# Kernel optimization log

Hardware: AMD Instinct MI355X
Metric: run time of the kernel (lower is better)

The kernel has to match this reference:

```python
import jax, jax.numpy as jnp
import numpy as np

N, T, D, H = 32, 2048, 256, 256


def setup_inputs() -> dict:
    key = jax.random.key(0)
    k0, k1, k2, k3, k4 = jax.random.split(key, 5)
    std = 1.0 / np.sqrt(H + D)  # matches PTLSTM.reset()
    return {
        "x": jax.random.normal(k0, (N, T, D), dtype=jnp.float32),
        "state": jnp.zeros((N, 2 * H), dtype=jnp.float32),  # [h0 | c0]
        "w_ih": (jax.random.normal(k1, (4 * H, D)) * std).astype(jnp.float32),
        "w_hh": (jax.random.normal(k2, (4 * H, H)) * std).astype(jnp.float32),
        "b_ih": (jax.random.normal(k3, (4 * H,)) * std).astype(jnp.float32),
        "b_hh": (jax.random.normal(k4, (4 * H,)) * std).astype(jnp.float32),
    }


def reference(x, state, w_ih, w_hh, b_ih, b_hh):
    # Single-layer batch_first LSTM, PyTorch gate order (i, f, g, o).
    Hd = w_hh.shape[1]
    h0, c0 = state[:, :Hd], state[:, Hd:]
    # Precompute input-to-hidden projection for all timesteps (one big GEMM).
    xg = jnp.einsum('ntd,gd->ntg', x, w_ih) + (b_ih + b_hh)  # [N, T, 4H]

    def step(carry, xg_t):
        h, c = carry
        gates = xg_t + h @ w_hh.T  # [N, 4H]
        i, f, g, o = jnp.split(gates, 4, axis=-1)
        i = jax.nn.sigmoid(i)
        f = jax.nn.sigmoid(f)
        g = jnp.tanh(g)
        o = jax.nn.sigmoid(o)
        c = f * c + i * g
        h = o * jnp.tanh(c)
        return (h, c), h

    (hT, cT), out_t = jax.lax.scan(step, (h0, c0), jnp.swapaxes(xg, 0, 1))
    output = jnp.swapaxes(out_t, 0, 1)  # [N, T, H]
    outstate = jnp.concatenate([hT, cT], axis=1)  # [N, 2H]
    return output, outstate
```

## Files before the change

kernel.cpp:

```cpp
#include <hip/hip_runtime.h>

typedef _Float16 half2_t __attribute__((ext_vector_type(2)));
typedef __bf16   bf16x8  __attribute__((ext_vector_type(8)));
typedef float    f32x4   __attribute__((ext_vector_type(4)));
typedef unsigned short u16x8 __attribute__((ext_vector_type(8)));
typedef unsigned int  uint32;
typedef unsigned long long uint64;

#define LSTM_N 32
#define LSTM_T 2048
#define LSTM_D 256
#define LSTM_H 256
#define NG 1024
#define CH 256
#define NCH (LSTM_T / CH)
#define MCH (LSTM_N * CH)

#define OFF_XG   ((size_t)0)
#define SZ_XG    ((size_t)MCH * NG * 4)
#define OFF_WIHB (OFF_XG + SZ_XG)
#define SZ_WIHB  ((size_t)NG * LSTM_D * 2)
#define OFF_BIAS (OFF_WIHB + SZ_WIHB)
#define SZ_BIAS  ((size_t)4096)
#define OFF_WPK  (OFF_BIAS + SZ_BIAS)
#define SZ_WPK   ((size_t)4 * 512 * 64 * 4)
#define OFF_CST  (OFF_WPK + SZ_WPK)
#define SZ_CST   ((size_t)LSTM_N * 256 * 4)
#define OFF_HX   (OFF_CST + SZ_CST)
#define SZ_HX    ((size_t)LSTM_N * 2 * 128 * 8)

#if defined(__has_builtin)
#if __has_builtin(__builtin_amdgcn_fdot2)
#define HAVE_FDOT2 1
#endif
#endif

__device__ __forceinline__ float fdot2(uint32 w, uint32 h, float acc) {
#ifdef HAVE_FDOT2
  return __builtin_amdgcn_fdot2(__builtin_bit_cast(half2_t, w),
                                __builtin_bit_cast(half2_t, h), acc, false);
#else
  half2_t wv = __builtin_bit_cast(half2_t, w);
  half2_t hv = __builtin_bit_cast(half2_t, h);
  float r = fmaf((float)wv.x, (float)hv.x, acc);
  return fmaf((float)wv.y, (float)hv.y, r);
#endif
}

__device__ __forceinline__ float sigm(float x) { return 1.f / (1.f + __expf(-x)); }
__device__ __forceinline__ float tanh_fast(float x) { return 2.f / (1.f + __expf(-2.f * x)) - 1.f; }

__device__ __forceinline__ unsigned short f2bf(float f) {
  uint32 u = __builtin_bit_cast(uint32, f);
  uint32 r = (u + 0x7FFFu + ((u >> 16) & 1u)) >> 16;
  return (unsigned short)r;
}

__device__ __forceinline__ float bfly8(const float a[8], int kap) {
  float k0[4], g0[4];
  const bool b4 = (kap & 4) != 0;
#pragma unroll
  for (int v = 0; v < 4; ++v) {
    k0[v] = b4 ? a[v + 4] : a[v];
    g0[v] = b4 ? a[v] : a[v + 4];
  }
#pragma unroll
  for (int v = 0; v < 4; ++v) k0[v] += __shfl_xor(g0[v], 4, 64);
  float k1[2], g1[2];
  const bool b2 = (kap & 2) != 0;
#pragma unroll
  for (int v = 0; v < 2; ++v) {
    k1[v] = b2 ? k0[v + 2] : k0[v];
    g1[v] = b2 ? k0[v] : k0[v + 2];
  }
#pragma unroll
  for (int v = 0; v < 2; ++v) k1[v] += __shfl_xor(g1[v], 2, 64);
  const bool b1 = (kap & 1) != 0;
  float k2 = b1 ? k1[1] : k1[0];
  float g2 = b1 ? k1[0] : k1[1];
  return k2 + __shfl_xor(g2, 1, 64);
}


__global__ void cvt_bf16_k(const float* __restrict__ src, unsigned short* __restrict__ dst, int n) {
  int i = blockIdx.x * blockDim.x + threadIdx.x;
  if (4 * i + 3 < n) {
    float4 v = ((const float4*)src)[i];
    ushort4 o;
    o.x = f2bf(v.x); o.y = f2bf(v.y); o.z = f2bf(v.z); o.w = f2bf(v.w);
    ((ushort4*)dst)[i] = o;
  }
}

__global__ void bias_sum_k(const float* __restrict__ bih, const float* __restrict__ bhh,
                           float* __restrict__ bias) {
  int g = blockIdx.x * blockDim.x + threadIdx.x;
  if (g < NG) bias[g] = bih[g] + bhh[g];
}

__global__ void wpack_k(const float* __restrict__ whh, uint32* __restrict__ wpk) {
  int e = blockIdx.x * blockDim.x + threadIdx.x;
  int j = e >> 15;
  int rem = e & 32767;
  int i = rem >> 9;
  int t = rem & 511;
  int kap = t & 15, rg = t >> 4;
  int rho = 8 * rg + (i >> 3);
  int R = (rho >> 6) * 256 + 64 * j + (rho & 63);
  int k = 16 * kap + 2 * (i & 7);
  half2_t h;
  h.x = (_Float16)whh[R * 256 + k];
  h.y = (_Float16)whh[R * 256 + k + 1];
  wpk[((j * 16 + (i >> 2)) * 512 + t) * 4 + (i & 3)] = __builtin_bit_cast(uint32, h);
}

__global__ void state_init_k(const float* __restrict__ state, float* __restrict__ cst,
                             uint64* __restrict__ hx) {
  int i = blockIdx.x * blockDim.x + threadIdx.x;
  int n = i >> 8, jj = i & 255;
  cst[i] = state[n * 512 + 256 + jj];
  if (jj < 128) {
    half2_t h2;
    h2.x = (_Float16)state[n * 512 + 2 * jj];
    h2.y = (_Float16)state[n * 512 + 2 * jj + 1];
    hx[(size_t)n * 256 + jj] = (uint64)__builtin_bit_cast(uint32, h2);
  } else {
    hx[(size_t)n * 256 + jj] = 0x8000000000000000ull;
  }
}

__global__ __launch_bounds__(256) void gemm_xg(const float* __restrict__ x,
                                               const unsigned short* __restrict__ wb,
                                               const float* __restrict__ bias,
                                               float* __restrict__ xg, int ch) {
  __shared__ unsigned short As[128 * 40];
  __shared__ unsigned short Bs[128 * 40];
  const int tid = threadIdx.x;
  const int m0 = blockIdx.y * 128;
  const int g0 = blockIdx.x * 128;
  const int w = tid >> 6;
  const int lane = tid & 63;
  const int wm = (w >> 1) * 64, wn = (w & 1) * 64;
  const int row_l = tid >> 2;
  const int q = tid & 3;
  const int lr = lane & 15, kg = lane >> 4;

  size_t grow[2];
#pragma unroll
  for (int r = 0; r < 2; ++r) {
    int gm = m0 + row_l + 64 * r;
    grow[r] = (size_t)(gm >> 8) * LSTM_T + (size_t)ch * CH + (gm & 255);
  }

  f32x4 acc[4][4];
#pragma unroll
  for (int i = 0; i < 4; ++i)
#pragma unroll
    for (int j = 0; j < 4; ++j) acc[i][j] = (f32x4){0.f, 0.f, 0.f, 0.f};

  for (int kt = 0; kt < 8; ++kt) {
#pragma unroll
    for (int r = 0; r < 2; ++r) {
      int row = row_l + 64 * r;
      const float* ap = x + grow[r] * 256 + kt * 32 + q * 8;
      float4 v0 = *(const float4*)ap;
      float4 v1 = *(const float4*)(ap + 4);
      u16x8 o;
      o[0] = f2bf(v0.x); o[1] = f2bf(v0.y); o[2] = f2bf(v0.z); o[3] = f2bf(v0.w);
      o[4] = f2bf(v1.x); o[5] = f2bf(v1.y); o[6] = f2bf(v1.z); o[7] = f2bf(v1.w);
      *(uint4*)((char*)As + row * 80 + q * 16) = __builtin_bit_cast(uint4, o);
      uint4 bv = *(const uint4*)(wb + (size_t)(g0 + row) * 256 + kt * 32 + q * 8);
      *(uint4*)((char*)Bs + row * 80 + q * 16) = bv;
    }
    __syncthreads();
    bf16x8 af[4], bfr[4];
#pragma unroll
    for (int i = 0; i < 4; ++i)
      af[i] = __builtin_bit_cast(bf16x8, *(const uint4*)((char*)As + (wm + 16 * i + lr) * 80 + kg * 16));
#pragma unroll
    for (int j = 0; j < 4; ++j)
      bfr[j] = __builtin_bit_cast(bf16x8, *(const uint4*)((char*)Bs + (wn + 16 * j + lr) * 80 + kg * 16));
#pragma unroll
    for (int i = 0; i < 4; ++i)
#pragma unroll
      for (int j = 0; j < 4; ++j)
        acc[i][j] = __builtin_amdgcn_mfma_f32_16x16x32_bf16(af[i], bfr[j], acc[i][j], 0, 0, 0);
    __syncthreads();
  }
#pragma unroll
  for (int j = 0; j < 4; ++j) {
    int gc = g0 + wn + 16 * j + lr;
    float bj = bias[gc];
#pragma unroll
    for (int i = 0; i < 4; ++i) {
#pragma unroll
      for (int r = 0; r < 4; ++r) {
        int m = m0 + wm + 16 * i + kg * 4 + r;
        xg[(size_t)m * NG + gc] = acc[i][j][r] + bj;
      }
    }
  }
}

__global__ __launch_bounds__(512, 1) void lstm_scan(const float* __restrict__ xg,
                                                    const uint4* __restrict__ wpk4,
                                                    float* __restrict__ cst,
                                                    uint64* __restrict__ hx,
                                                    float* __restrict__ out, int ch) {
  __shared__ uint32 hb[2][128];
  __shared__ float actb[256];
  __shared__ float ostage[16][64];

  const int b = blockIdx.x;
  const int n = b & 31;
  const int j = b >> 5;
  const int t = threadIdx.x;
  const int kap = t & 15;
  const int rg = t >> 4;
  const int rho_f = 8 * rg + (t & 7);
  const int qf = rho_f >> 6;
  const int Rf = qf * 256 + 64 * j + (rho_f & 63);

  uint32 wr[64];
#pragma unroll
  for (int ig = 0; ig < 16; ++ig) {
    uint4 v = wpk4[(j * 16 + ig) * 512 + t];
    wr[4 * ig + 0] = v.x; wr[4 * ig + 1] = v.y; wr[4 * ig + 2] = v.z; wr[4 * ig + 3] = v.w;
  }
  float c = 0.f;
  if (t < 64) c = cst[n * 256 + 64 * j + t];

  const float* xgn = xg + (size_t)n * CH * NG;
  float* outb = out + ((size_t)n * LSTM_T + (size_t)ch * CH) * LSTM_H;
  uint64* board = hx + (size_t)n * 256;
  const int gsbase = ch * CH;

  float xcur = xgn[Rf];

  for (int tt = 0; tt < CH; ++tt) {
    const int s = gsbase + tt;
    const int par = s & 1;
    if (t < 128 && (tt == 0 || (t >> 5) != j)) {
      uint64* sp = &board[(size_t)par * 128 + t];
      uint64 v;
      for (;;) {
        v = __hip_atomic_load(sp, __ATOMIC_RELAXED, __HIP_MEMORY_SCOPE_AGENT);
        if ((uint32)(v >> 32) == (uint32)s) break;
        __builtin_amdgcn_s_sleep(1);
      }
      hb[par][t] = (uint32)v;
    }
    __syncthreads();
    uint32 hh[8];
    *(uint4*)&hh[0] = *(const uint4*)&hb[par][8 * kap];
    *(uint4*)&hh[4] = *(const uint4*)&hb[par][8 * kap + 4];
    float acc[8];
#pragma unroll
    for (int r = 0; r < 8; ++r) {
      float a = 0.f;
#pragma unroll
      for (int m = 0; m < 8; ++m) a = fdot2(wr[r * 8 + m], hh[m], a);
      acc[r] = a;
    }
#pragma unroll
    for (int r = 0; r < 8; ++r) acc[r] += __shfl_xor(acc[r], 8, 64);
    float ssum = bfly8(acc, t & 7);
    float pre = ssum + xcur;
    if (tt < CH - 1) xcur = xgn[(size_t)(tt + 1) * NG + Rf];
    float a = (qf == 2) ? tanh_fast(pre) : sigm(pre);
    if (kap < 8) actb[rho_f] = a;
    __syncthreads();
    if (t < 64) {
      float gi = actb[t];
      float gf = actb[64 + t];
      float gg = actb[128 + t];
      float go = actb[192 + t];
      c = gf * c + gi * gg;
      float h = go * tanh_fast(c);
      _Float16 hf = (_Float16)h;
      uint32 hz = (uint32)__builtin_bit_cast(unsigned short, hf);
      ((unsigned short*)&hb[par ^ 1][0])[64 * j + t] = (unsigned short)hz;
      ostage[tt & 15][t] = h;
      uint32 hn = (uint32)__shfl_xor((int)hz, 1, 64);
      if ((t & 1) == 0) {
        uint64 msg = (uint64)(hz | (hn << 16)) | ((uint64)(uint32)(s + 1) << 32);
        __hip_atomic_store(&board[(size_t)((s + 1) & 1) * 128 + 32 * j + (t >> 1)],
                           msg, __ATOMIC_RELAXED, __HIP_MEMORY_SCOPE_AGENT);
      }
      if (ch == NCH - 1 && tt == CH - 1) {
        float* os = out + (size_t)LSTM_N * LSTM_T * LSTM_H + n * 512;
        os[64 * j + t] = h;
        os[256 + 64 * j + t] = c;
      }
    }
    if ((tt & 15) == 15) {
      __syncthreads();
      if (t < 256) {
        int sl = t >> 4, c4 = t & 15;
        float4 v = *(const float4*)&ostage[sl][4 * c4];
        *(float4*)&outb[(size_t)(tt - 15 + sl) * LSTM_H + 64 * j + 4 * c4] = v;
      }
    }
  }
  if (t < 64) cst[n * 256 + 64 * j + t] = c;
}

extern "C" void kernel_launch(void* const* d_in, const int* in_sizes, int n_in,
                              void* d_out, int out_size, void* d_ws, size_t ws_size,
                              hipStream_t stream) {
  const float* x   = (const float*)d_in[0];
  const float* st  = (const float*)d_in[1];
  const float* wih = (const float*)d_in[2];
  const float* whh = (const float*)d_in[3];
  const float* bih = (const float*)d_in[4];
  const float* bhh = (const float*)d_in[5];
  float* out = (float*)d_out;
  char* ws = (char*)d_ws;

  float* xg = (float*)(ws + OFF_XG);
  unsigned short* wihb = (unsigned short*)(ws + OFF_WIHB);
  float* bias = (float*)(ws + OFF_BIAS);
  uint32* wpk = (uint32*)(ws + OFF_WPK);
  float* cst = (float*)(ws + OFF_CST);
  uint64* hx = (uint64*)(ws + OFF_HX);

  cvt_bf16_k<<<(NG * LSTM_D / 4 + 255) / 256, 256, 0, stream>>>(wih, wihb, NG * LSTM_D);
  bias_sum_k<<<4, 256, 0, stream>>>(bih, bhh, bias);
  wpack_k<<<512, 256, 0, stream>>>(whh, wpk);
  state_init_k<<<32, 256, 0, stream>>>(st, cst, hx);

  for (int ch = 0; ch < NCH; ++ch) {
    gemm_xg<<<dim3(NG / 128, MCH / 128), 256, 0, stream>>>(x, wihb, bias, xg, ch);
    lstm_scan<<<128, 512, 0, stream>>>(xg, (const uint4*)wpk, cst, hx, out, ch);
  }
}
```

Measured before the change: 3.289 ms.

## Split LSTM recurrence across 8 hidden slices per block, interleave two sequences

Each scan block now owns 32 hidden units (8 blocks per sequence instead of 4) and handles two batch sequences back to back, so each thread holds half as many recurrent weights and a 4-lane reduction replaces the 16-lane butterfly. Interleaving the two sequences is meant to hide cross-block handshake latency for one sequence behind compute for the other. In exchange, each block waits on more blocks per step, runs more barriers per timestep, and has less dot-product work per thread to cover latency. The launch-side grid size is not shown.

```diff
diff --git a/kernel.cpp b/kernel.cpp
--- a/kernel.cpp
+++ b/kernel.cpp
@@ -23,7 +23,7 @@
 #define OFF_BIAS (OFF_WIHB + SZ_WIHB)
 #define SZ_BIAS  ((size_t)4096)
 #define OFF_WPK  (OFF_BIAS + SZ_BIAS)
-#define SZ_WPK   ((size_t)4 * 512 * 64 * 4)
+#define SZ_WPK   ((size_t)8 * 512 * 32 * 4)
 #define OFF_CST  (OFF_WPK + SZ_WPK)
 #define SZ_CST   ((size_t)LSTM_N * 256 * 4)
 #define OFF_HX   (OFF_CST + SZ_CST)
@@ -56,31 +56,6 @@
   return (unsigned short)r;
 }
 
-__device__ __forceinline__ float bfly8(const float a[8], int kap) {
-  float k0[4], g0[4];
-  const bool b4 = (kap & 4) != 0;
-#pragma unroll
-  for (int v = 0; v < 4; ++v) {
-    k0[v] = b4 ? a[v + 4] : a[v];
-    g0[v] = b4 ? a[v] : a[v + 4];
-  }
-#pragma unroll
-  for (int v = 0; v < 4; ++v) k0[v] += __shfl_xor(g0[v], 4, 64);
-  float k1[2], g1[2];
-  const bool b2 = (kap & 2) != 0;
-#pragma unroll
-  for (int v = 0; v < 2; ++v) {
-    k1[v] = b2 ? k0[v + 2] : k0[v];
-    g1[v] = b2 ? k0[v] : k0[v + 2];
-  }
-#pragma unroll
-  for (int v = 0; v < 2; ++v) k1[v] += __shfl_xor(g1[v], 2, 64);
-  const bool b1 = (kap & 1) != 0;
-  float k2 = b1 ? k1[1] : k1[0];
-  float g2 = b1 ? k1[0] : k1[1];
-  return k2 + __shfl_xor(g2, 1, 64);
-}
-
 
 __global__ void cvt_bf16_k(const float* __restrict__ src, unsigned short* __restrict__ dst, int n) {
   int i = blockIdx.x * blockDim.x + threadIdx.x;
@@ -99,19 +74,17 @@
 }
 
 __global__ void wpack_k(const float* __restrict__ whh, uint32* __restrict__ wpk) {
-  int e = blockIdx.x * blockDim.x + threadIdx.x;
-  int j = e >> 15;
-  int rem = e & 32767;
-  int i = rem >> 9;
-  int t = rem & 511;
-  int kap = t & 15, rg = t >> 4;
-  int rho = 8 * rg + (i >> 3);
-  int R = (rho >> 6) * 256 + 64 * j + (rho & 63);
-  int k = 16 * kap + 2 * (i & 7);
+  int idx = blockIdx.x * blockDim.x + threadIdx.x;
+  int e = idx >> 14;
+  int m = (idx >> 9) & 31;
+  int t = idx & 511;
+  int r_loc = t >> 2, kq = t & 3;
+  int R = (r_loc >> 5) * 256 + 32 * e + (r_loc & 31);
+  int k = 64 * kq + 2 * m;
   half2_t h;
   h.x = (_Float16)whh[R * 256 + k];
   h.y = (_Float16)whh[R * 256 + k + 1];
-  wpk[((j * 16 + (i >> 2)) * 512 + t) * 4 + (i & 3)] = __builtin_bit_cast(uint32, h);
+  wpk[((e * 8 + (m >> 2)) * 512 + t) * 4 + (m & 3)] = __builtin_bit_cast(uint32, h);
 }
 
 __global__ void state_init_k(const float* __restrict__ state, float* __restrict__ cst,
@@ -207,102 +180,164 @@
                                                     float* __restrict__ cst,
                                                     uint64* __restrict__ hx,
                                                     float* __restrict__ out, int ch) {
-  __shared__ uint32 hb[2][128];
-  __shared__ float actb[256];
-  __shared__ float ostage[16][64];
+  __shared__ uint32 hbA[2][128];
+  __shared__ uint32 hbB[2][128];
+  __shared__ float actb[128];
+  __shared__ float ostage[2][16][32];
 
   const int b = blockIdx.x;
-  const int n = b & 31;
-  const int j = b >> 5;
+  const int g = (b & 7) | ((b >> 6) << 3);
+  const int e = (b >> 3) & 7;
+  const int nA = 2 * g, nB = 2 * g + 1;
   const int t = threadIdx.x;
-  const int kap = t & 15;
-  const int rg = t >> 4;
-  const int rho_f = 8 * rg + (t & 7);
-  const int qf = rho_f >> 6;
-  const int Rf = qf * 256 + 64 * j + (rho_f & 63);
-
-  uint32 wr[64];
-#pragma unroll
-  for (int ig = 0; ig < 16; ++ig) {
-    uint4 v = wpk4[(j * 16 + ig) * 512 + t];
+  const int r_loc = t >> 2, kq = t & 3;
+  const int q = r_loc >> 5, u_loc = r_loc & 31;
+  const int R = q * 256 + 32 * e + u_loc;
+
+  uint32 wr[32];
+#pragma unroll
+  for (int ig = 0; ig < 8; ++ig) {
+    uint4 v = wpk4[(e * 8 + ig) * 512 + t];
     wr[4 * ig + 0] = v.x; wr[4 * ig + 1] = v.y; wr[4 * ig + 2] = v.z; wr[4 * ig + 3] = v.w;
   }
-  float c = 0.f;
-  if (t < 64) c = cst[n * 256 + 64 * j + t];
-
-  const float* xgn = xg + (size_t)n * CH * NG;
-  float* outb = out + ((size_t)n * LSTM_T + (size_t)ch * CH) * LSTM_H;
-  uint64* board = hx + (size_t)n * 256;
+  float cA = 0.f, cB = 0.f;
+  if (t < 32) {
+    cA = cst[nA * 256 + 32 * e + t];
+    cB = cst[nB * 256 + 32 * e + t];
+  }
+
+  const float* xgA = xg + (size_t)nA * CH * NG;
+  const float* xgB = xg + (size_t)nB * CH * NG;
+  float* outA = out + ((size_t)nA * LSTM_T + (size_t)ch * CH) * LSTM_H + 32 * e;
+  float* outB = out + ((size_t)nB * LSTM_T + (size_t)ch * CH) * LSTM_H + 32 * e;
+  uint64* boardA = hx + (size_t)nA * 256;
+  uint64* boardB = hx + (size_t)nB * 256;
   const int gsbase = ch * CH;
-
-  float xcur = xgn[Rf];
 
   for (int tt = 0; tt < CH; ++tt) {
     const int s = gsbase + tt;
     const int par = s & 1;
-    if (t < 128 && (tt == 0 || (t >> 5) != j)) {
-      uint64* sp = &board[(size_t)par * 128 + t];
+    float xcA = 0.f;
+    if (kq == 0) xcA = xgA[(size_t)tt * NG + R];
+    if (t < 128 && (tt == 0 || (t >> 4) != e)) {
+      uint64* sp = &boardA[(size_t)par * 128 + t];
       uint64 v;
       for (;;) {
         v = __hip_atomic_load(sp, __ATOMIC_RELAXED, __HIP_MEMORY_SCOPE_AGENT);
         if ((uint32)(v >> 32) == (uint32)s) break;
         __builtin_amdgcn_s_sleep(1);
       }
-      hb[par][t] = (uint32)v;
-    }
-    __syncthreads();
-    uint32 hh[8];
-    *(uint4*)&hh[0] = *(const uint4*)&hb[par][8 * kap];
-    *(uint4*)&hh[4] = *(const uint4*)&hb[par][8 * kap + 4];
-    float acc[8];
-#pragma unroll
-    for (int r = 0; r < 8; ++r) {
-      float a = 0.f;
-#pragma unroll
-      for (int m = 0; m < 8; ++m) a = fdot2(wr[r * 8 + m], hh[m], a);
-      acc[r] = a;
-    }
-#pragma unroll
-    for (int r = 0; r < 8; ++r) acc[r] += __shfl_xor(acc[r], 8, 64);
-    float ssum = bfly8(acc, t & 7);
-    float pre = ssum + xcur;
-    if (tt < CH - 1) xcur = xgn[(size_t)(tt + 1) * NG + Rf];
-    float a = (qf == 2) ? tanh_fast(pre) : sigm(pre);
-    if (kap < 8) actb[rho_f] = a;
-    __syncthreads();
-    if (t < 64) {
-      float gi = actb[t];
-      float gf = actb[64 + t];
-      float gg = actb[128 + t];
-      float go = actb[192 + t];
-      c = gf * c + gi * gg;
-      float h = go * tanh_fast(c);
+      hbA[par][t] = (uint32)v;
+    }
+    __syncthreads();
+    {
+      const uint4* hb4 = (const uint4*)&hbA[par][32 * kq];
+      uint32 hh[32];
+#pragma unroll
+      for (int i = 0; i < 8; ++i) *(uint4*)&hh[4 * i] = hb4[i];
+      float a0 = 0.f, a1 = 0.f;
+#pragma unroll
+      for (int m = 0; m < 16; ++m) {
+        a0 = fdot2(wr[2 * m], hh[2 * m], a0);
+        a1 = fdot2(wr[2 * m + 1], hh[2 * m + 1], a1);
+      }
+      float a = a0 + a1;
+      a += __shfl_xor(a, 1, 64);
+      a += __shfl_xor(a, 2, 64);
+      if (kq == 0) {
+        float pre = a + xcA;
+        actb[r_loc] = (q == 2) ? tanh_fast(pre) : sigm(pre);
+      }
+    }
+    __syncthreads();
+    if (t < 32) {
+      float gi = actb[t], gf = actb[32 + t], gg = actb[64 + t], go = actb[96 + t];
+      cA = gf * cA + gi * gg;
+      float h = go * tanh_fast(cA);
       _Float16 hf = (_Float16)h;
       uint32 hz = (uint32)__builtin_bit_cast(unsigned short, hf);
-      ((unsigned short*)&hb[par ^ 1][0])[64 * j + t] = (unsigned short)hz;
-      ostage[tt & 15][t] = h;
+      ((unsigned short*)&hbA[par ^ 1][0])[32 * e + t] = (unsigned short)hz;
+      ostage[0][tt & 15][t] = h;
       uint32 hn = (uint32)__shfl_xor((int)hz, 1, 64);
       if ((t & 1) == 0) {
         uint64 msg = (uint64)(hz | (hn << 16)) | ((uint64)(uint32)(s + 1) << 32);
-        __hip_atomic_store(&board[(size_t)((s + 1) & 1) * 128 + 32 * j + (t >> 1)],
+        __hip_atomic_store(&boardA[(size_t)((s + 1) & 1) * 128 + 16 * e + (t >> 1)],
                            msg, __ATOMIC_RELAXED, __HIP_MEMORY_SCOPE_AGENT);
       }
       if (ch == NCH - 1 && tt == CH - 1) {
-        float* os = out + (size_t)LSTM_N * LSTM_T * LSTM_H + n * 512;
-        os[64 * j + t] = h;
-        os[256 + 64 * j + t] = c;
+        float* os = out + (size_t)LSTM_N * LSTM_T * LSTM_H + nA * 512;
+        os[32 * e + t] = h;
+        os[256 + 32 * e + t] = cA;
+      }
+    }
+    float xcB = 0.f;
+    if (kq == 0) xcB = xgB[(size_t)tt * NG + R];
+    if (t < 128 && (tt == 0 || (t >> 4) != e)) {
+      uint64* sp = &boardB[(size_t)par * 128 + t];
+      uint64 v;
+      for (;;) {
+        v = __hip_atomic_load(sp, __ATOMIC_RELAXED, __HIP_MEMORY_SCOPE_AGENT);
+        if ((uint32)(v >> 32) == (uint32)s) break;
+        __builtin_amdgcn_s_sleep(1);
+      }
+      hbB[par][t] = (uint32)v;
+    }
+    __syncthreads();
+    {
+      const uint4* hb4 = (const uint4*)&hbB[par][32 * kq];
+      uint32 hh[32];
+#pragma unroll
+      for (int i = 0; i < 8; ++i) *(uint4*)&hh[4 * i] = hb4[i];
+      float a0 = 0.f, a1 = 0.f;
+#pragma unroll
+      for (int m = 0; m < 16; ++m) {
+        a0 = fdot2(wr[2 * m], hh[2 * m], a0);
+        a1 = fdot2(wr[2 * m + 1], hh[2 * m + 1], a1);
+      }
+      float a = a0 + a1;
+      a += __shfl_xor(a, 1, 64);
+      a += __shfl_xor(a, 2, 64);
+      if (kq == 0) {
+        float pre = a + xcB;
+        actb[r_loc] = (q == 2) ? tanh_fast(pre) : sigm(pre);
+      }
+    }
+    __syncthreads();
+    if (t < 32) {
+      float gi = actb[t], gf = actb[32 + t], gg = actb[64 + t], go = actb[96 + t];
+      cB = gf * cB + gi * gg;
+      float h = go * tanh_fast(cB);
+      _Float16 hf = (_Float16)h;
+      uint32 hz = (uint32)__builtin_bit_cast(unsigned short, hf);
+      ((unsigned short*)&hbB[par ^ 1][0])[32 * e + t] = (unsigned short)hz;
+      ostage[1][tt & 15][t] = h;
+      uint32 hn = (uint32)__shfl_xor((int)hz, 1, 64);
+      if ((t & 1) == 0) {
+        uint64 msg = (uint64)(hz | (hn << 16)) | ((uint64)(uint32)(s + 1) << 32);
+        __hip_atomic_store(&boardB[(size_t)((s + 1) & 1) * 128 + 16 * e + (t >> 1)],
+                           msg, __ATOMIC_RELAXED, __HIP_MEMORY_SCOPE_AGENT);
+      }
+      if (ch == NCH - 1 && tt == CH - 1) {
+        float* os = out + (size_t)LSTM_N * LSTM_T * LSTM_H + nB * 512;
+        os[32 * e + t] = h;
+        os[256 + 32 * e + t] = cB;
       }
     }
     if ((tt & 15) == 15) {
       __syncthreads();
       if (t < 256) {
-        int sl = t >> 4, c4 = t & 15;
-        float4 v = *(const float4*)&ostage[sl][4 * c4];
-        *(float4*)&outb[(size_t)(tt - 15 + sl) * LSTM_H + 64 * j + 4 * c4] = v;
-      }
-    }
-  }
-  if (t < 64) cst[n * 256 + 64 * j + t] = c;
+        int ph = t >> 7, r = t & 127;
+        int sl = r >> 3, li = r & 7;
+        float4 v = *(const float4*)&ostage[ph][sl][4 * li];
+        float* ob = ph ? outB : outA;
+        *(float4*)&ob[(size_t)(tt - 15 + sl) * LSTM_H + 4 * li] = v;
+      }
+    }
+  }
+  if (t < 32) {
+    cst[nA * 256 + 32 * e + t] = cA;
+    cst[nB * 256 + 32 * e + t] = cB;
+  }
 }
 
 extern "C" void kernel_launch(void* const* d_in, const int* in_sizes, int n_in,
```

Measured after the change: 4.704 ms. 1.43x slower.
